# Optimization experiments

Hardware: AMD Instinct MI355X
Metric: run time of the kernel (lower is better)

## Reference

```python
import jax, jax.numpy as jnp
import numpy as np

N_NODES = 50000
NUM_REL = 8
IN_DIM = 128
HID = 256
NUM_CLASSES = 2
E = 1600000
M = 200000
LN_EPS = 1e-5


def setup_inputs() -> dict:
    key = jax.random.key(0)
    ks = jax.random.split(key, 20)
    s = 0.05
    inp = {
        "x": jax.random.normal(ks[0], (N_NODES, IN_DIM), jnp.float32),
        "edge_index": jax.random.randint(ks[1], (2, E), 0, N_NODES, jnp.int32),
        "edge_type": jax.random.randint(ks[2], (E,), 0, NUM_REL, jnp.int32),
        "dec_edges": jax.random.randint(ks[3], (M, 2), 0, N_NODES, jnp.int32),
        # conv1
        "W1": jax.random.normal(ks[4], (NUM_REL, IN_DIM, HID), jnp.float32) * s,
        "root1": jax.random.normal(ks[5], (IN_DIM, HID), jnp.float32) * s,
        "b1": jnp.zeros((HID,), jnp.float32),
        # conv2
        "W2": jax.random.normal(ks[6], (NUM_REL, HID, HID), jnp.float32) * s,
        "root2": jax.random.normal(ks[7], (HID, HID), jnp.float32) * s,
        "b2": jnp.zeros((HID,), jnp.float32),
        # layernorms
        "ln1_g": jnp.ones((HID,), jnp.float32),
        "ln1_b": jnp.zeros((HID,), jnp.float32),
        "ln2_g": jnp.ones((HID,), jnp.float32),
        "ln2_b": jnp.zeros((HID,), jnp.float32),
        # edge MLP: 2*HID -> HID -> HID//2 -> NUM_CLASSES
        "mlp_w1": jax.random.normal(ks[8], (2 * HID, HID), jnp.float32) * s,
        "mlp_b1": jnp.zeros((HID,), jnp.float32),
        "mlp_w2": jax.random.normal(ks[9], (HID, HID // 2), jnp.float32) * s,
        "mlp_b2": jnp.zeros((HID // 2,), jnp.float32),
        "mlp_w3": jax.random.normal(ks[10], (HID // 2, NUM_CLASSES), jnp.float32) * s,
        "mlp_b3": jnp.zeros((NUM_CLASSES,), jnp.float32),
    }
    return inp


def layer_norm(h, g, b):
    mu = jnp.mean(h, axis=-1, keepdims=True)
    var = jnp.mean(jnp.square(h - mu), axis=-1, keepdims=True)
    return (h - mu) * jax.lax.rsqrt(var + LN_EPS) * g + b


def rgcn_conv(x, edge_index, edge_type, W, root, bias):
    # PyG RGCNConv with aggr='mean': per-relation mean aggregation of
    # neighbor features, aggregate-then-transform (valid since linear),
    # plus root transform and bias.
    src, dst = edge_index[0], edge_index[1]
    xs = x[src]  # [E, d_in]
    out = x @ root + bias
    num_rel = W.shape[0]
    for r in range(num_rel):
        m = (edge_type == r).astype(x.dtype)  # [E]
        agg = jax.ops.segment_sum(xs * m[:, None], dst, num_segments=x.shape[0])
        cnt = jax.ops.segment_sum(m, dst, num_segments=x.shape[0])
        out = out + (agg / jnp.maximum(cnt, 1.0)[:, None]) @ W[r]
    return out


def reference(x, edge_index, edge_type, dec_edges,
              W1, root1, b1, W2, root2, b2,
              ln1_g, ln1_b, ln2_g, ln2_b,
              mlp_w1, mlp_b1, mlp_w2, mlp_b2, mlp_w3, mlp_b3):
    # encode (dropout is identity in eval mode)
    h1 = rgcn_conv(x, edge_index, edge_type, W1, root1, b1)
    h1 = layer_norm(jax.nn.relu(h1), ln1_g, ln1_b)
    h2 = rgcn_conv(h1, edge_index, edge_type, W2, root2, b2)
    h2 = layer_norm(jax.nn.relu(h2), ln2_g, ln2_b)
    h = h1 + h2
    # decode: gather endpoints, concat, MLP (exact-erf GELU as nn.GELU)
    z = jnp.concatenate([h[dec_edges[:, 0]], h[dec_edges[:, 1]]], axis=1)
    z = jax.nn.gelu(z @ mlp_w1 + mlp_b1, approximate=False)
    z = jax.nn.gelu(z @ mlp_w2 + mlp_b2, approximate=False)
    return z @ mlp_w3 + mlp_b3
```

## Files before the change

kernel.cpp:

```cpp
#include <hip/hip_runtime.h>
#include <math.h>

typedef __attribute__((ext_vector_type(8))) short short8;
typedef __attribute__((ext_vector_type(4))) float f32x4;
typedef __attribute__((address_space(3))) void lds_void;
typedef const __attribute__((address_space(1))) void glb_void;

#define N_NODES 50000
#define NUM_REL 8
#define IN_DIM 128
#define HID 256
#define E_EDGES 1600000
#define M_DEC 200000
#define K1 1152
#define K2 2304
#define LN_EPS 1e-5f
#define NSEG (N_NODES * 8)
#define NB2 782
#define SA_WG 391
#define SA_CH 4096
#define SA_DCH 512

#define RFL(x) __builtin_amdgcn_readfirstlane(x)

__device__ __forceinline__ float b2f(ushort u) {
    union { unsigned int i; float f; } v; v.i = ((unsigned int)u) << 16; return v.f;
}
__device__ __forceinline__ ushort f2b(float f) {
    union { float f; unsigned int i; } v; v.f = f;
    unsigned int r = v.i + 0x7FFFu + ((v.i >> 16) & 1u);
    return (ushort)(r >> 16);
}
__device__ __forceinline__ unsigned int pk2(ushort a, ushort b) {
    return (unsigned int)a | ((unsigned int)b << 16);
}
__device__ __forceinline__ float gelu_fast(float x) {
    float y = 1.5957691216f * (x + 0.044715f * x * x * x);
    float e = __expf(y);
    float t = 1.f - 2.f * __builtin_amdgcn_rcpf(e + 1.f);
    return 0.5f * x * (1.f + t);
}
__device__ __forceinline__ int clampn(int v) {
    if ((unsigned)v >= N_NODES) v = (v < 0) ? 0 : N_NODES - 1;
    return v;
}


__global__ __launch_bounds__(256) void coarse_count(const int* __restrict__ ei,
                                                    const int* __restrict__ dec,
                                                    int* __restrict__ bh, int* __restrict__ dh) {
    __shared__ int lb[NB2], ld[NB2];
    const int t = threadIdx.x;
    for (int i = t; i < NB2; i += 256) { lb[i] = 0; ld[i] = 0; }
    __syncthreads();
    const int e0 = blockIdx.x * SA_CH;
#pragma unroll
    for (int k = 0; k < 16; ++k) {
        int e = e0 + k * 256 + t;
        if (e < E_EDGES) {
            int dst = clampn(ei[E_EDGES + e]);
            atomicAdd(&lb[dst >> 6], 1);
        }
    }
    const int d0 = blockIdx.x * SA_DCH;
#pragma unroll
    for (int k = 0; k < 2; ++k) {
        int i = d0 + k * 256 + t;
        if (i < M_DEC) {
            int a = clampn(dec[(size_t)i * 2]);
            atomicAdd(&ld[a >> 6], 1);
        }
    }
    __syncthreads();
    for (int i = t; i < NB2; i += 256) {
        if (lb[i]) atomicAdd(&bh[i], lb[i]);
        if (ld[i]) atomicAdd(&dh[i], ld[i]);
    }
}

__global__ __launch_bounds__(1024) void scan_buckets(const int* __restrict__ bh, int* __restrict__ bbase,
                                                     int* __restrict__ bcur,
                                                     const int* __restrict__ dh, int* __restrict__ dbase,
                                                     int* __restrict__ dcur, int* __restrict__ rp2) {
    __shared__ int ts[1024];
    const int t = threadIdx.x;
    const int* src = (blockIdx.x == 0) ? bh : dh;
    int* ob = (blockIdx.x == 0) ? bbase : dbase;
    int* oc = (blockIdx.x == 0) ? bcur : dcur;
    int v = (t < NB2) ? src[t] : 0;
    ts[t] = v;
    __syncthreads();
#pragma unroll
    for (int off = 1; off < 1024; off <<= 1) {
        int u = (t >= off) ? ts[t - off] : 0;
        __syncthreads();
        ts[t] += u;
        __syncthreads();
    }
    if (t < NB2) { int ex = ts[t] - v; ob[t] = ex; oc[t] = ex; }
    if (t == NB2 - 1) ob[NB2] = ts[t];
    if (t == 0 && blockIdx.x == 0) rp2[NSEG] = E_EDGES;
}

__global__ __launch_bounds__(256) void stageA(const int* __restrict__ ei, const int* __restrict__ et,
                                              int* __restrict__ bcur, unsigned int* __restrict__ sbuf,
                                              const int* __restrict__ dec, int* __restrict__ dcur,
                                              int* __restrict__ perm) {
    __shared__ int h[NB2], base_[NB2];
    const int t = threadIdx.x;
    const int e0 = blockIdx.x * SA_CH;
    for (int i = t; i < NB2; i += 256) h[i] = 0;
    __syncthreads();
    int myb[16];
#pragma unroll
    for (int k = 0; k < 16; ++k) {
        int e = e0 + k * 256 + t;
        int b = -1;
        if (e < E_EDGES) {
            int dst = clampn(ei[E_EDGES + e]);
            b = dst >> 6;
            atomicAdd(&h[b], 1);
        }
        myb[k] = b;
    }
    __syncthreads();
    for (int i = t; i < NB2; i += 256) {
        int c = h[i];
        base_[i] = c ? atomicAdd(&bcur[i], c) : 0;
    }
    __syncthreads();
    for (int i = t; i < NB2; i += 256) h[i] = 0;
    __syncthreads();
#pragma unroll
    for (int k = 0; k < 16; ++k) {
        int e = e0 + k * 256 + t;
        int b = myb[k];
        if (b >= 0) {
            int dst = clampn(ei[E_EDGES + e]);
            int src = clampn(ei[e]);
            int r = et[e] & 7;
            int off = atomicAdd(&h[b], 1);
            sbuf[base_[b] + off] =
                (unsigned)src | ((unsigned)r << 16) | ((unsigned)(dst & 63) << 19);
        }
    }
    __syncthreads();
    for (int i = t; i < NB2; i += 256) h[i] = 0;
    __syncthreads();
    const int d0 = blockIdx.x * SA_DCH;
    int dbk[2];
#pragma unroll
    for (int k = 0; k < 2; ++k) {
        int i = d0 + k * 256 + t;
        int b = -1;
        if (i < M_DEC) {
            int a = clampn(dec[(size_t)i * 2]);
            b = a >> 6;
            atomicAdd(&h[b], 1);
        }
        dbk[k] = b;
    }
    __syncthreads();
    for (int i = t; i < NB2; i += 256) {
        int c = h[i];
        base_[i] = c ? atomicAdd(&dcur[i], c) : 0;
    }
    __syncthreads();
    for (int i = t; i < NB2; i += 256) h[i] = 0;
    __syncthreads();
#pragma unroll
    for (int k = 0; k < 2; ++k) {
        int i = d0 + k * 256 + t;
        int b = dbk[k];
        if (b >= 0) {
            int off = atomicAdd(&h[b], 1);
            perm[base_[b] + off] = i;
        }
    }
}

__global__ __launch_bounds__(512) void stageB(const unsigned int* __restrict__ sbuf,
                                              const int* __restrict__ bbase,
                                              int* __restrict__ rp2,
                                              unsigned int* __restrict__ epk) {
    __shared__ int cnt[512];
    __shared__ int pref[512];
    const int t = threadIdx.x;
    const int b = blockIdx.x;
    const int s0 = bbase[b], s1 = bbase[b + 1];
    cnt[t] = 0;
    __syncthreads();
    for (int i = s0 + t; i < s1; i += 512) {
        unsigned int p = sbuf[i];
        int ls = (((p >> 19) & 63) << 3) | ((p >> 16) & 7);
        atomicAdd(&cnt[ls], 1);
    }
    __syncthreads();
    pref[t] = cnt[t];
    __syncthreads();
#pragma unroll
    for (int off = 1; off < 512; off <<= 1) {
        int u = (t >= off) ? pref[t - off] : 0;
        __syncthreads();
        pref[t] += u;
        __syncthreads();
    }
    int excl = pref[t] - cnt[t];
    int seg = b * 512 + t;
    if (seg < NSEG) rp2[seg] = s0 + excl;
    __syncthreads();
    pref[t] = excl;
    cnt[t] = 0;
    __syncthreads();
    for (int i = s0 + t; i < s1; i += 512) {
        unsigned int p = sbuf[i];
        int ls = (((p >> 19) & 63) << 3) | ((p >> 16) & 7);
        int off = atomicAdd(&cnt[ls], 1);
        epk[s0 + pref[ls] + off] = p & 0xFFFFu;
    }
}

__global__ void pack_all(const float* __restrict__ x, ushort* __restrict__ xb,
                         const float* __restrict__ root1, const float* __restrict__ W1,
                         const float* __restrict__ root2, const float* __restrict__ W2,
                         ushort* __restrict__ B1t, ushort* __restrict__ B2t,
                         const float* __restrict__ mw1, const float* __restrict__ mw2,
                         ushort* __restrict__ wuvt, ushort* __restrict__ w2t) {
    const int XC = N_NODES * IN_DIM / 4;
    const int N1 = HID * K1;
    const int N2 = HID * K2;
    const int NU = 512 * 256;
    const int NW = 128 * 256;
    int idx = blockIdx.x * 256 + threadIdx.x;
    if (idx < XC) {
        float4 v = *(const float4*)(x + (size_t)idx * 4);
        uint2 o;
        o.x = pk2(f2b(v.x), f2b(v.y));
        o.y = pk2(f2b(v.z), f2b(v.w));
        *(uint2*)(xb + (size_t)idx * 4) = o;
        return;
    }
    idx -= XC;
    if (idx < N1) {
        int n = idx / K1, k = idx % K1;
        float v;
        if (k < IN_DIM) v = root1[k * HID + n];
        else { int kk = k - IN_DIM; v = W1[(size_t)(kk >> 7) * IN_DIM * HID + (kk & 127) * HID + n]; }
        B1t[(size_t)n * K1 + k] = f2b(v);
        return;
    }
    idx -= N1;
    if (idx < N2) {
        int n = idx / K2, k = idx % K2;
        float v;
        if (k < HID) v = root2[k * HID + n];
        else { int kk = k - HID; v = W2[(size_t)(kk >> 8) * HID * HID + (kk & 255) * HID + n]; }
        B2t[(size_t)n * K2 + k] = f2b(v);
        return;
    }
    idx -= N2;
    if (idx < NU) {
        int n = idx / 256, k = idx % 256;
        float v = (n < 256) ? mw1[(size_t)k * 256 + n] : mw1[(size_t)(256 + k) * 256 + (n - 256)];
        wuvt[(size_t)n * 256 + k] = f2b(v);
        return;
    }
    idx -= NU;
    if (idx < NW) {
        int n = idx / 256, k = idx % 256;
        w2t[n * 256 + k] = f2b(mw2[k * 128 + n]);
    }
}


#define FL1() { int c_ = segend - segbeg; float inv_ = c_ > 0 ? 1.f / (float)c_ : 0.f; \
    *(unsigned int*)(Arow + IN_DIM + r * IN_DIM + 2 * lane) = \
        pk2(f2b((aA.x + aB.x) * inv_), f2b((aA.y + aB.y) * inv_)); \
    aA.x = 0.f; aA.y = 0.f; aB.x = 0.f; aB.y = 0.f; \
    ++r; segbeg = segend; segend = (r < 8) ? RFL(rp[r + 1]) : end; \
    if (segend < segbeg) segend = segbeg; if (segend > end) segend = end; }
#define CK1(EI) { while (r < 8 && (EI) >= segend) FL1(); }
#define AC1A(U) { aA.x += b2f((ushort)((U) & 0xFFFFu)); aA.y += b2f((ushort)((U) >> 16)); }
#define AC1B(U) { aB.x += b2f((ushort)((U) & 0xFFFFu)); aB.y += b2f((ushort)((U) >> 16)); }

__global__ __launch_bounds__(256) void agg1_kernel(const ushort* __restrict__ xb,
                                                   const int* __restrict__ rp2,
                                                   const unsigned int* __restrict__ epk,
                                                   ushort* __restrict__ Achunk, int n0, int m) {
    const int w = threadIdx.x >> 6, lane = threadIdx.x & 63;
    const int local = blockIdx.x * 4 + w;
    if (local >= m) return;
    const int n = n0 + local;
    const int* rp = rp2 + n * 8;
    ushort* Arow = Achunk + (size_t)local * K1;
    const ushort* xbb = xb + 2 * lane;
    *(unsigned int*)(Arow + 2 * lane) = *(const unsigned int*)(xb + (size_t)n * IN_DIM + 2 * lane);

    int beg = RFL(rp[0]), end = RFL(rp[8]);
    if (beg < 0) beg = 0;
    if (end > E_EDGES) end = E_EDGES;
    if (end < beg) end = beg;

    float2 aA = {0.f, 0.f}, aB = {0.f, 0.f};
    int r = 0, segbeg = beg, segend = RFL(rp[1]);
    if (segend < segbeg) segend = segbeg; if (segend > end) segend = end;

    int e = beg;
    for (; e + 7 < end; e += 8) {
        unsigned int p0 = RFL(epk[e]),     p1 = RFL(epk[e + 1]);
        unsigned int p2 = RFL(epk[e + 2]), p3 = RFL(epk[e + 3]);
        unsigned int p4 = RFL(epk[e + 4]), p5 = RFL(epk[e + 5]);
        unsigned int p6 = RFL(epk[e + 6]), p7 = RFL(epk[e + 7]);
        unsigned int u0 = *(const unsigned int*)(xbb + (size_t)p0 * IN_DIM);
        unsigned int u1 = *(const unsigned int*)(xbb + (size_t)p1 * IN_DIM);
        unsigned int u2 = *(const unsigned int*)(xbb + (size_t)p2 * IN_DIM);
        unsigned int u3 = *(const unsigned int*)(xbb + (size_t)p3 * IN_DIM);
        unsigned int u4 = *(const unsigned int*)(xbb + (size_t)p4 * IN_DIM);
        unsigned int u5 = *(const unsigned int*)(xbb + (size_t)p5 * IN_DIM);
        unsigned int u6 = *(const unsigned int*)(xbb + (size_t)p6 * IN_DIM);
        unsigned int u7 = *(const unsigned int*)(xbb + (size_t)p7 * IN_DIM);
        CK1(e)     AC1A(u0) CK1(e + 1) AC1B(u1)
        CK1(e + 2) AC1A(u2) CK1(e + 3) AC1B(u3)
        CK1(e + 4) AC1A(u4) CK1(e + 5) AC1B(u5)
        CK1(e + 6) AC1A(u6) CK1(e + 7) AC1B(u7)
    }
    for (; e < end; ++e) {
        unsigned int p = RFL(epk[e]);
        unsigned int u = *(const unsigned int*)(xbb + (size_t)p * IN_DIM);
        CK1(e) AC1A(u)
    }
    while (r < 8) FL1();
}

#define FL2() { int c_ = segend - segbeg; float inv_ = c_ > 0 ? 1.f / (float)c_ : 0.f; \
    f32x4 t_ = aA + aB; uint2 o_; \
    o_.x = pk2(f2b(t_[0] * inv_), f2b(t_[1] * inv_)); \
    o_.y = pk2(f2b(t_[2] * inv_), f2b(t_[3] * inv_)); \
    *(uint2*)(Arow + HID + r * HID + 4 * lane) = o_; \
    aA = (f32x4){0.f, 0.f, 0.f, 0.f}; aB = aA; \
    ++r; segbeg = segend; segend = (r < 8) ? RFL(rp[r + 1]) : end; \
    if (segend < segbeg) segend = segbeg; if (segend > end) segend = end; }
#define CK2(EI) { while (r < 8 && (EI) >= segend) FL2(); }
#define AC2A(U) { f32x4 f_; \
    f_[0] = b2f((ushort)((U).x & 0xFFFFu)); f_[1] = b2f((ushort)((U).x >> 16)); \
    f_[2] = b2f((ushort)((U).y & 0xFFFFu)); f_[3] = b2f((ushort)((U).y >> 16)); aA += f_; }
#define AC2B(U) { f32x4 f_; \
    f_[0] = b2f((ushort)((U).x & 0xFFFFu)); f_[1] = b2f((ushort)((U).x >> 16)); \
    f_[2] = b2f((ushort)((U).y & 0xFFFFu)); f_[3] = b2f((ushort)((U).y >> 16)); aB += f_; }

__global__ __launch_bounds__(256) void agg2_kernel(const ushort* __restrict__ h1,
                                                   const int* __restrict__ rp2,
                                                   const unsigned int* __restrict__ epk,
                                                   ushort* __restrict__ Achunk, int n0, int m) {
    const int w = threadIdx.x >> 6, lane = threadIdx.x & 63;
    const int local = blockIdx.x * 4 + w;
    if (local >= m) return;
    const int n = n0 + local;
    const int* rp = rp2 + n * 8;
    ushort* Arow = Achunk + (size_t)local * K2;
    const ushort* hb = h1 + 4 * lane;
    *(uint2*)(Arow + 4 * lane) = *(const uint2*)(h1 + (size_t)n * HID + 4 * lane);

    int beg = RFL(rp[0]), end = RFL(rp[8]);
    if (beg < 0) beg = 0;
    if (end > E_EDGES) end = E_EDGES;
    if (end < beg) end = beg;

    f32x4 aA = {0.f, 0.f, 0.f, 0.f}, aB = {0.f, 0.f, 0.f, 0.f};
    int r = 0, segbeg = beg, segend = RFL(rp[1]);
    if (segend < segbeg) segend = segbeg; if (segend > end) segend = end;

    int e = beg;
    for (; e + 7 < end; e += 8) {
        unsigned int p0 = RFL(epk[e]),     p1 = RFL(epk[e + 1]);
        unsigned int p2 = RFL(epk[e + 2]), p3 = RFL(epk[e + 3]);
        unsigned int p4 = RFL(epk[e + 4]), p5 = RFL(epk[e + 5]);
        unsigned int p6 = RFL(epk[e + 6]), p7 = RFL(epk[e + 7]);
        uint2 u0 = *(const uint2*)(hb + (size_t)p0 * HID);
        uint2 u1 = *(const uint2*)(hb + (size_t)p1 * HID);
        uint2 u2 = *(const uint2*)(hb + (size_t)p2 * HID);
        uint2 u3 = *(const uint2*)(hb + (size_t)p3 * HID);
        uint2 u4 = *(const uint2*)(hb + (size_t)p4 * HID);
        uint2 u5 = *(const uint2*)(hb + (size_t)p5 * HID);
        uint2 u6 = *(const uint2*)(hb + (size_t)p6 * HID);
        uint2 u7 = *(const uint2*)(hb + (size_t)p7 * HID);
        CK2(e)     AC2A(u0) CK2(e + 1) AC2B(u1)
        CK2(e + 2) AC2A(u2) CK2(e + 3) AC2B(u3)
        CK2(e + 4) AC2A(u4) CK2(e + 5) AC2B(u5)
        CK2(e + 6) AC2A(u6) CK2(e + 7) AC2B(u7)
    }
    for (; e < end; ++e) {
        unsigned int p = RFL(epk[e]);
        uint2 u = *(const uint2*)(hb + (size_t)p * HID);
        CK2(e) AC2A(u)
    }
    while (r < 8) FL2();
}


#define STAGE(BUF, KO) { \
    __builtin_amdgcn_global_load_lds((glb_void*)(Ab + (KO)), \
        (lds_void*)(AsBase + (BUF) * 4096 + wave * 8 * 64), 16, 0, 0); \
    _Pragma("unroll") \
    for (int j_ = 0; j_ < 4; ++j_) \
        __builtin_amdgcn_global_load_lds((glb_void*)(Bb + (size_t)j_ * 8 * K + (KO)), \
            (lds_void*)(BsBase + (BUF) * 16384 + (wave * 32 + j_ * 8) * 64), 16, 0, 0); }

#define COMPUTE(CUR) { \
    _Pragma("unroll") \
    for (int kk = 0; kk < 2; ++kk) { \
        const int gsw = (((kk * 4 + qd) ^ (cc & 7)) * 8); \
        short8 af[2], bfv[4]; \
        _Pragma("unroll") \
        for (int i = 0; i < 2; ++i) \
            af[i] = *(const short8*)&AsBase[(CUR) * 4096 + (mh * 32 + i * 16 + cc) * 64 + gsw]; \
        _Pragma("unroll") \
        for (int j = 0; j < 4; ++j) \
            bfv[j] = *(const short8*)&BsBase[(CUR) * 16384 + (wn + j * 16 + cc) * 64 + gsw]; \
        _Pragma("unroll") \
        for (int i = 0; i < 2; ++i) \
            _Pragma("unroll") \
            for (int j = 0; j < 4; ++j) \
                acc[i][j] = __builtin_amdgcn_mfma_f32_16x16x32_bf16(af[i], bfv[j], acc[i][j], 0, 0, 0); \
    } }

__global__ __launch_bounds__(512, 4) void gemm_fused(
    const ushort* __restrict__ A, const ushort* __restrict__ Bt,
    int lda, int M, int K,
    const float* __restrict__ bias, const float* __restrict__ g,
    const float* __restrict__ bvec, const ushort* __restrict__ resid,
    ushort* __restrict__ outp, int ldc, int rowOff) {
    __shared__ __align__(16) ushort smem[40960];
    ushort* AsBase = smem;
    ushort* BsBase = smem + 2 * 64 * 64;
    const int tid = threadIdx.x;
    const int wave = tid >> 6, lane = tid & 63;
    const int w4 = wave & 3, mh = wave >> 2;
    const int cc = lane & 15, qd = lane >> 4;
    const int row0 = blockIdx.x * 64;
    const int colBase = blockIdx.y * 256;
    const int wn = w4 * 64;
    const int srow = lane >> 3;
    const int sgrp = (lane & 7) ^ (srow & 7);
    f32x4 acc[2][4];
#pragma unroll
    for (int i = 0; i < 2; ++i)
#pragma unroll
        for (int j = 0; j < 4; ++j) acc[i][j] = (f32x4){0.f, 0.f, 0.f, 0.f};

    const ushort* Ab = A + (size_t)(row0 + wave * 8 + srow) * lda + sgrp * 8;
    const ushort* Bb = Bt + (size_t)(colBase + wave * 32 + srow) * K + sgrp * 8;

    STAGE(0, 0)
    for (int k0 = 0; k0 < K; k0 += 128) {
        if (k0 + 64 < K) {
            STAGE(1, k0 + 64)
            asm volatile("s_waitcnt vmcnt(5)" ::: "memory");
        } else {
            asm volatile("s_waitcnt vmcnt(0)" ::: "memory");
        }
        __builtin_amdgcn_s_barrier();
        COMPUTE(0)
        asm volatile("s_waitcnt lgkmcnt(0)" ::: "memory");
        __builtin_amdgcn_s_barrier();

        if (k0 + 128 < K) {
            STAGE(0, k0 + 128)
            asm volatile("s_waitcnt vmcnt(5)" ::: "memory");
        } else {
            asm volatile("s_waitcnt vmcnt(0)" ::: "memory");
        }
        __builtin_amdgcn_s_barrier();
        COMPUTE(1)
        asm volatile("s_waitcnt lgkmcnt(0)" ::: "memory");
        __builtin_amdgcn_s_barrier();
    }

    if (g) {
        float* partS = (float*)smem;
        float* partQ = (float*)smem + 256;
        float* muS   = (float*)smem + 512;
        float* rsS   = (float*)smem + 576;
#pragma unroll
        for (int j = 0; j < 4; ++j) {
            float bcol = bias[wn + j * 16 + cc];
#pragma unroll
            for (int i = 0; i < 2; ++i)
#pragma unroll
                for (int r = 0; r < 4; ++r)
                    acc[i][j][r] = fmaxf(acc[i][j][r] + bcol, 0.f);
        }
#pragma unroll
        for (int i = 0; i < 2; ++i)
#pragma unroll
            for (int r = 0; r < 4; ++r) {
                float s = acc[i][0][r] + acc[i][1][r] + acc[i][2][r] + acc[i][3][r];
                float q = acc[i][0][r] * acc[i][0][r] + acc[i][1][r] * acc[i][1][r]
                        + acc[i][2][r] * acc[i][2][r] + acc[i][3][r] * acc[i][3][r];
#pragma unroll
                for (int off = 1; off <= 8; off <<= 1) {
                    s += __shfl_xor(s, off, 64);
                    q += __shfl_xor(q, off, 64);
                }
                if (cc == 0) {
                    int row = mh * 32 + i * 16 + qd * 4 + r;
                    partS[row * 4 + w4] = s;
                    partQ[row * 4 + w4] = q;
                }
            }
        __syncthreads();
        if (tid < 64) {
            float S = partS[tid * 4] + partS[tid * 4 + 1] + partS[tid * 4 + 2] + partS[tid * 4 + 3];
            float Q = partQ[tid * 4] + partQ[tid * 4 + 1] + partQ[tid * 4 + 2] + partQ[tid * 4 + 3];
            float mu = S * (1.f / 256.f);
            float var = Q * (1.f / 256.f) - mu * mu;
            muS[tid] = mu;
            rsS[tid] = rsqrtf(fmaxf(var, 0.f) + LN_EPS);
        }
        __syncthreads();
#pragma unroll
        for (int i = 0; i < 2; ++i)
#pragma unroll
            for (int r = 0; r < 4; ++r) {
                int row = mh * 32 + i * 16 + qd * 4 + r;
                int grow = row0 + row;
                if (grow >= M) continue;
                float mu = muS[row], rs = rsS[row];
                size_t base = (size_t)(rowOff + grow) * ldc;
#pragma unroll
                for (int j = 0; j < 4; ++j) {
                    int col = wn + j * 16 + cc;
                    float val = (acc[i][j][r] - mu) * rs * g[col] + bvec[col];
                    if (resid) val += b2f(resid[base + col]);
                    outp[base + col] = f2b(val);
                }
            }
    } else {
#pragma unroll
        for (int i = 0; i < 2; ++i)
#pragma unroll
            for (int r = 0; r < 4; ++r) {
                int grow = row0 + mh * 32 + i * 16 + qd * 4 + r;
                if (grow >= M) continue;
                size_t base = (size_t)(rowOff + grow) * ldc;
#pragma unroll
                for (int j = 0; j < 4; ++j) {
                    int col = colBase + wn + j * 16 + cc;
                    outp[base + col] = f2b(acc[i][j][r]);
                }
            }
    }
}

__global__ __launch_bounds__(256) void edge_kernel(
    const ushort* __restrict__ uv, const int* __restrict__ dec, const int* __restrict__ perm,
    const float* __restrict__ b1, const ushort* __restrict__ w2t,
    const float* __restrict__ b2, const float* __restrict__ w3,
    const float* __restrict__ b3, float* __restrict__ outp, int M) {
    __shared__ __align__(16) ushort z1s[64][264];
    __shared__ __align__(16) ushort z2s[64][136];
    __shared__ float b1s[256], b2s[128], w3s[256];
    __shared__ float part3[64][2][2];
    const int tid = threadIdx.x;
    const int wave = tid >> 6, lane = tid & 63;
    const int cc = lane & 15, qd = lane >> 4, lk = qd * 8, rr = qd * 4;
    const int e0 = blockIdx.x * 64;

    b1s[tid] = b1[tid];
    if (tid < 128) b2s[tid] = b2[tid];
    w3s[tid] = w3[tid];
    __syncthreads();

    {
        int e = tid >> 2, seg = tid & 3;
        int ge = perm[e0 + e];
        if (ge < 0) ge = 0; if (ge >= M) ge = M - 1;
        int a = dec[(size_t)ge * 2];
        int b = dec[(size_t)ge * 2 + 1];
        if (a < 0) a = 0; if (a >= N_NODES) a = N_NODES - 1;
        if (b < 0) b = 0; if (b >= N_NODES) b = N_NODES - 1;
        const ushort* up = uv + (size_t)a * 512 + seg * 64;
        const ushort* vp = uv + (size_t)b * 512 + 256 + seg * 64;
        short8 us[8], vs[8];
#pragma unroll
        for (int j = 0; j < 8; ++j) us[j] = *(const short8*)(up + j * 8);
#pragma unroll
        for (int j = 0; j < 8; ++j) vs[j] = *(const short8*)(vp + j * 8);
        int d0 = seg * 64;
#pragma unroll
        for (int j = 0; j < 8; ++j) {
            int d = d0 + j * 8;
            short8 zs;
#pragma unroll
            for (int l = 0; l < 8; ++l) {
                float z = b2f((ushort)us[j][l]) + b2f((ushort)vs[j][l]) + b1s[d + l];
                zs[l] = (short)f2b(gelu_fast(z));
            }
            *(short8*)&z1s[e][d] = zs;
        }
    }
    __syncthreads();

    f32x4 acc[4][2];
#pragma unroll
    for (int i = 0; i < 4; ++i)
#pragma unroll
        for (int j = 0; j < 2; ++j) acc[i][j] = (f32x4){0.f, 0.f, 0.f, 0.f};
    const int n0 = wave * 32;
#pragma unroll
    for (int ks = 0; ks < 8; ++ks) {
        short8 af[4], bfv[2];
#pragma unroll
        for (int i = 0; i < 4; ++i) af[i] = *(const short8*)&z1s[i * 16 + cc][ks * 32 + lk];
#pragma unroll
        for (int j = 0; j < 2; ++j)
            bfv[j] = *(const short8*)(w2t + (size_t)(n0 + j * 16 + cc) * 256 + ks * 32 + lk);
#pragma unroll
        for (int i = 0; i < 4; ++i)
#pragma unroll
            for (int j = 0; j < 2; ++j)
                acc[i][j] = __builtin_amdgcn_mfma_f32_16x16x32_bf16(af[i], bfv[j], acc[i][j], 0, 0, 0);
    }
#pragma unroll
    for (int i = 0; i < 4; ++i)
#pragma unroll
        for (int j = 0; j < 2; ++j)
#pragma unroll
            for (int r = 0; r < 4; ++r) {
                int m = i * 16 + rr + r;
                int n = n0 + j * 16 + cc;
                z2s[m][n] = f2b(gelu_fast(acc[i][j][r] + b2s[n]));
            }
    __syncthreads();

    {
        int e = tid >> 2, c = tid & 1, hf = (tid >> 1) & 1;
        const ushort* zr = &z2s[e][hf * 64];
        float s = 0.f;
#pragma unroll
        for (int j = 0; j < 8; ++j) {
            short8 v = *(const short8*)(zr + j * 8);
#pragma unroll
            for (int l = 0; l < 8; ++l)
                s += b2f((ushort)v[l]) * w3s[(hf * 64 + j * 8 + l) * 2 + c];
        }
        part3[e][c][hf] = s;
    }
    __syncthreads();
    if (tid < 128) {
        int e = tid >> 1, c = tid & 1;
        float s = part3[e][c][0] + part3[e][c][1] + b3[c];
        int ge = perm[e0 + e];
        if (ge >= 0 && ge < M) outp[(size_t)ge * 2 + c] = s;
    }
}

extern "C" void kernel_launch(void* const* d_in, const int* in_sizes, int n_in,
                              void* d_out, int out_size, void* d_ws, size_t ws_size,
                              hipStream_t stream) {
    const float* x          = (const float*)d_in[0];
    const int*   edge_index = (const int*)d_in[1];
    const int*   edge_type  = (const int*)d_in[2];
    const int*   dec_edges  = (const int*)d_in[3];
    const float* W1         = (const float*)d_in[4];
    const float* root1      = (const float*)d_in[5];
    const float* b1         = (const float*)d_in[6];
    const float* W2         = (const float*)d_in[7];
    const float* root2      = (const float*)d_in[8];
    const float* b2         = (const float*)d_in[9];
    const float* ln1_g      = (const float*)d_in[10];
    const float* ln1_b      = (const float*)d_in[11];
    const float* ln2_g      = (const float*)d_in[12];
    const float* ln2_b      = (const float*)d_in[13];
    const float* mlp_w1     = (const float*)d_in[14];
    const float* mlp_b1     = (const float*)d_in[15];
    const float* mlp_w2     = (const float*)d_in[16];
    const float* mlp_b2     = (const float*)d_in[17];
    const float* mlp_w3     = (const float*)d_in[18];
    const float* mlp_b3     = (const float*)d_in[19];

    char* ws = (char*)d_ws;
    size_t off = 0;
    auto alloc = [&](size_t bytes) {
        void* p = ws + off;
        off += (bytes + 255) & ~(size_t)255;
        return p;
    };
    unsigned int* epk     = (unsigned int*)alloc((size_t)E_EDGES * 4);
    unsigned int* sbuf    = (unsigned int*)alloc((size_t)E_EDGES * 4);
    int*          rp2     = (int*)alloc((size_t)(NSEG + 1) * 4);
    int*          hz      = (int*)alloc((size_t)2 * NB2 * 4);
    int*          bh      = hz;
    int*          dh      = hz + NB2;
    int*          bbase   = (int*)alloc((size_t)(NB2 + 1) * 4);
    int*          dbase   = (int*)alloc((size_t)(NB2 + 1) * 4);
    int*          bcur    = (int*)alloc((size_t)NB2 * 4);
    int*          dcur    = (int*)alloc((size_t)NB2 * 4);
    int*          perm    = (int*)alloc((size_t)M_DEC * 4);
    ushort*       B1t     = (ushort*)alloc((size_t)HID * K1 * 2);
    ushort*       B2t     = (ushort*)alloc((size_t)HID * K2 * 2);
    ushort*       wuvt    = (ushort*)alloc((size_t)512 * 256 * 2);
    ushort*       w2t     = (ushort*)alloc((size_t)128 * 256 * 2);
    ushort*       xb      = (ushort*)alloc((size_t)N_NODES * IN_DIM * 2);
    ushort*       hfin    = (ushort*)alloc((size_t)N_NODES * HID * 2);

    size_t regionOff = off;
    ushort* h1ln  = (ushort*)(ws + regionOff);
    ushort* uvbuf = h1ln;
    size_t h1b = (((size_t)N_NODES * HID * 2) + 255) & ~(size_t)255;
    ushort* Achunk = (ushort*)(ws + regionOff + h1b);
    long long chunkB = (long long)ws_size - (long long)(regionOff + h1b);
    int chunk = 64;
    if (chunkB > 0) {
        long long c = chunkB / ((long long)K2 * 2);
        if (c > N_NODES) c = N_NODES;
        c &= ~63LL;
        if (c >= 64) chunk = (int)c;
    }
    int chunk1 = chunk * 2;
    if (chunk1 > N_NODES) chunk1 = N_NODES;

    hipMemsetAsync(hz, 0, (size_t)2 * NB2 * 4, stream);
    coarse_count<<<SA_WG, 256, 0, stream>>>(edge_index, dec_edges, bh, dh);
    scan_buckets<<<2, 1024, 0, stream>>>(bh, bbase, bcur, dh, dbase, dcur, rp2);
    stageA<<<SA_WG, 256, 0, stream>>>(edge_index, edge_type, bcur, sbuf, dec_edges, dcur, perm);
    stageB<<<NB2, 512, 0, stream>>>(sbuf, bbase, rp2, epk);

    {
        int total = N_NODES * IN_DIM / 4 + HID * K1 + HID * K2 + 512 * 256 + 128 * 256;
        pack_all<<<(total + 255) / 256, 256, 0, stream>>>(x, xb, root1, W1, root2, W2,
                                                          B1t, B2t, mlp_w1, mlp_w2, wuvt, w2t);
    }

    for (int n0 = 0; n0 < N_NODES; n0 += chunk1) {
        int m = N_NODES - n0; if (m > chunk1) m = chunk1;
        agg1_kernel<<<(m + 3) / 4, 256, 0, stream>>>(xb, rp2, epk, Achunk, n0, m);
        gemm_fused<<<dim3((m + 63) / 64, 1), 512, 0, stream>>>(
            Achunk, B1t, K1, m, K1, b1, ln1_g, ln1_b, nullptr, h1ln, HID, n0);
    }
    for (int n0 = 0; n0 < N_NODES; n0 += chunk) {
        int m = N_NODES - n0; if (m > chunk) m = chunk;
        agg2_kernel<<<(m + 3) / 4, 256, 0, stream>>>(h1ln, rp2, epk, Achunk, n0, m);
        gemm_fused<<<dim3((m + 63) / 64, 1), 512, 0, stream>>>(
            Achunk, B2t, K2, m, K2, b2, ln2_g, ln2_b, h1ln, hfin, HID, n0);
    }

    gemm_fused<<<dim3((N_NODES + 63) / 64, 2), 512, 0, stream>>>(
        hfin, wuvt, HID, N_NODES, HID, nullptr, nullptr, nullptr, nullptr, uvbuf, 512, 0);

    edge_kernel<<<(M_DEC + 63) / 64, 256, 0, stream>>>(
        uvbuf, dec_edges, perm, mlp_b1, w2t, mlp_b2, mlp_w3, mlp_b3, (float*)d_out, M_DEC);
}
```

Before: 704.0 us.

## Double GEMM row tile to 128 so each B tile is reused across two A tiles

The fused GEMM now computes 128 rows per workgroup as two 64-row groups with separate accumulators. Each staged 64-column B tile is used by both groups, which halves B traffic per output row and halves the grid size. The load pipeline is rebuilt so A stages are interleaved with compute and B is prefetched two steps ahead, and A row indices are clamped at M. The cost is doubled accumulator registers and fewer workgroups, which may reduce occupancy and parallelism on small chunks.

```diff
diff --git a/kernel.cpp b/kernel.cpp
--- a/kernel.cpp
+++ b/kernel.cpp
@@ -398,30 +398,32 @@
 }
 
 
-#define STAGE(BUF, KO) { \
-    __builtin_amdgcn_global_load_lds((glb_void*)(Ab + (KO)), \
-        (lds_void*)(AsBase + (BUF) * 4096 + wave * 8 * 64), 16, 0, 0); \
+#define STAGEB(BUF, KO) { \
     _Pragma("unroll") \
     for (int j_ = 0; j_ < 4; ++j_) \
         __builtin_amdgcn_global_load_lds((glb_void*)(Bb + (size_t)j_ * 8 * K + (KO)), \
             (lds_void*)(BsBase + (BUF) * 16384 + (wave * 32 + j_ * 8) * 64), 16, 0, 0); }
 
-#define COMPUTE(CUR) { \
+#define STAGEA(G, PTR, KO) { \
+    __builtin_amdgcn_global_load_lds((glb_void*)((PTR) + (KO)), \
+        (lds_void*)(AsBase + (G) * 4096 + wave * 8 * 64), 16, 0, 0); }
+
+#define COMPUTEG(ACC, G, CB) { \
     _Pragma("unroll") \
     for (int kk = 0; kk < 2; ++kk) { \
         const int gsw = (((kk * 4 + qd) ^ (cc & 7)) * 8); \
         short8 af[2], bfv[4]; \
         _Pragma("unroll") \
         for (int i = 0; i < 2; ++i) \
-            af[i] = *(const short8*)&AsBase[(CUR) * 4096 + (mh * 32 + i * 16 + cc) * 64 + gsw]; \
+            af[i] = *(const short8*)&AsBase[(G) * 4096 + (mh * 32 + i * 16 + cc) * 64 + gsw]; \
         _Pragma("unroll") \
         for (int j = 0; j < 4; ++j) \
-            bfv[j] = *(const short8*)&BsBase[(CUR) * 16384 + (wn + j * 16 + cc) * 64 + gsw]; \
+            bfv[j] = *(const short8*)&BsBase[(CB) * 16384 + (wn + j * 16 + cc) * 64 + gsw]; \
         _Pragma("unroll") \
         for (int i = 0; i < 2; ++i) \
             _Pragma("unroll") \
             for (int j = 0; j < 4; ++j) \
-                acc[i][j] = __builtin_amdgcn_mfma_f32_16x16x32_bf16(af[i], bfv[j], acc[i][j], 0, 0, 0); \
+                ACC[i][j] = __builtin_amdgcn_mfma_f32_16x16x32_bf16(af[i], bfv[j], ACC[i][j], 0, 0, 0); \
     } }
 
 __global__ __launch_bounds__(512, 4) void gemm_fused(
@@ -437,79 +439,92 @@
     const int wave = tid >> 6, lane = tid & 63;
     const int w4 = wave & 3, mh = wave >> 2;
     const int cc = lane & 15, qd = lane >> 4;
-    const int row0 = blockIdx.x * 64;
+    const int row0 = blockIdx.x * 128;
     const int colBase = blockIdx.y * 256;
     const int wn = w4 * 64;
     const int srow = lane >> 3;
     const int sgrp = (lane & 7) ^ (srow & 7);
-    f32x4 acc[2][4];
+    f32x4 acc0[2][4], acc1[2][4];
 #pragma unroll
     for (int i = 0; i < 2; ++i)
 #pragma unroll
-        for (int j = 0; j < 4; ++j) acc[i][j] = (f32x4){0.f, 0.f, 0.f, 0.f};
-
-    const ushort* Ab = A + (size_t)(row0 + wave * 8 + srow) * lda + sgrp * 8;
+        for (int j = 0; j < 4; ++j) {
+            acc0[i][j] = (f32x4){0.f, 0.f, 0.f, 0.f};
+            acc1[i][j] = (f32x4){0.f, 0.f, 0.f, 0.f};
+        }
+
+    int rowA0 = row0 + wave * 8 + srow;       if (rowA0 >= M) rowA0 = M - 1;
+    int rowA1 = row0 + 64 + wave * 8 + srow;  if (rowA1 >= M) rowA1 = M - 1;
+    const ushort* Ab0 = A + (size_t)rowA0 * lda + sgrp * 8;
+    const ushort* Ab1 = A + (size_t)rowA1 * lda + sgrp * 8;
     const ushort* Bb = Bt + (size_t)(colBase + wave * 32 + srow) * K + sgrp * 8;
 
-    STAGE(0, 0)
-    for (int k0 = 0; k0 < K; k0 += 128) {
-        if (k0 + 64 < K) {
-            STAGE(1, k0 + 64)
-            asm volatile("s_waitcnt vmcnt(5)" ::: "memory");
-        } else {
-            asm volatile("s_waitcnt vmcnt(0)" ::: "memory");
-        }
+    const int NT = K >> 6;
+    STAGEB(0, 0)
+    STAGEA(0, Ab0, 0)
+    STAGEA(1, Ab1, 0)
+    if (NT > 1) STAGEB(1, 64)
+
+    for (int t = 0; t < NT; ++t) {
+        const int ko = t << 6;
+        const int cb = t & 1;
+        if (t + 1 < NT) { asm volatile("s_waitcnt vmcnt(5)" ::: "memory"); }
+        else           { asm volatile("s_waitcnt vmcnt(1)" ::: "memory"); }
         __builtin_amdgcn_s_barrier();
-        COMPUTE(0)
+        COMPUTEG(acc0, 0, cb)
         asm volatile("s_waitcnt lgkmcnt(0)" ::: "memory");
         __builtin_amdgcn_s_barrier();
-
-        if (k0 + 128 < K) {
-            STAGE(0, k0 + 128)
-            asm volatile("s_waitcnt vmcnt(5)" ::: "memory");
-        } else {
-            asm volatile("s_waitcnt vmcnt(0)" ::: "memory");
-        }
+        if (t + 1 < NT) STAGEA(0, Ab0, ko + 64)
+        if (t + 1 < NT) { asm volatile("s_waitcnt vmcnt(5)" ::: "memory"); }
+        else           { asm volatile("s_waitcnt vmcnt(0)" ::: "memory"); }
         __builtin_amdgcn_s_barrier();
-        COMPUTE(1)
+        COMPUTEG(acc1, 1, cb)
         asm volatile("s_waitcnt lgkmcnt(0)" ::: "memory");
         __builtin_amdgcn_s_barrier();
+        if (t + 1 < NT) {
+            STAGEA(1, Ab1, ko + 64)
+            if (t + 2 < NT) STAGEB(cb, ko + 128)
+        }
     }
 
     if (g) {
         float* partS = (float*)smem;
-        float* partQ = (float*)smem + 256;
-        float* muS   = (float*)smem + 512;
-        float* rsS   = (float*)smem + 576;
-#pragma unroll
-        for (int j = 0; j < 4; ++j) {
-            float bcol = bias[wn + j * 16 + cc];
+        float* partQ = (float*)smem + 512;
+        float* muS   = (float*)smem + 1024;
+        float* rsS   = (float*)smem + 1152;
+#pragma unroll
+        for (int gg = 0; gg < 2; ++gg) {
+            f32x4 (*ac)[4] = gg ? acc1 : acc0;
+#pragma unroll
+            for (int j = 0; j < 4; ++j) {
+                float bcol = bias[wn + j * 16 + cc];
+#pragma unroll
+                for (int i = 0; i < 2; ++i)
+#pragma unroll
+                    for (int r = 0; r < 4; ++r)
+                        ac[i][j][r] = fmaxf(ac[i][j][r] + bcol, 0.f);
+            }
 #pragma unroll
             for (int i = 0; i < 2; ++i)
 #pragma unroll
-                for (int r = 0; r < 4; ++r)
-                    acc[i][j][r] = fmaxf(acc[i][j][r] + bcol, 0.f);
-        }
-#pragma unroll
-        for (int i = 0; i < 2; ++i)
-#pragma unroll
-            for (int r = 0; r < 4; ++r) {
-                float s = acc[i][0][r] + acc[i][1][r] + acc[i][2][r] + acc[i][3][r];
-                float q = acc[i][0][r] * acc[i][0][r] + acc[i][1][r] * acc[i][1][r]
-                        + acc[i][2][r] * acc[i][2][r] + acc[i][3][r] * acc[i][3][r];
-#pragma unroll
-                for (int off = 1; off <= 8; off <<= 1) {
-                    s += __shfl_xor(s, off, 64);
-                    q += __shfl_xor(q, off, 64);
+                for (int r = 0; r < 4; ++r) {
+                    float s = ac[i][0][r] + ac[i][1][r] + ac[i][2][r] + ac[i][3][r];
+                    float q = ac[i][0][r] * ac[i][0][r] + ac[i][1][r] * ac[i][1][r]
+                            + ac[i][2][r] * ac[i][2][r] + ac[i][3][r] * ac[i][3][r];
+#pragma unroll
+                    for (int off = 1; off <= 8; off <<= 1) {
+                        s += __shfl_xor(s, off, 64);
+                        q += __shfl_xor(q, off, 64);
+                    }
+                    if (cc == 0) {
+                        int row = gg * 64 + mh * 32 + i * 16 + qd * 4 + r;
+                        partS[row * 4 + w4] = s;
+                        partQ[row * 4 + w4] = q;
+                    }
                 }
-                if (cc == 0) {
-                    int row = mh * 32 + i * 16 + qd * 4 + r;
-                    partS[row * 4 + w4] = s;
-                    partQ[row * 4 + w4] = q;
-                }
-            }
+        }
         __syncthreads();
-        if (tid < 64) {
+        if (tid < 128) {
             float S = partS[tid * 4] + partS[tid * 4 + 1] + partS[tid * 4 + 2] + partS[tid * 4 + 3];
             float Q = partQ[tid * 4] + partQ[tid * 4 + 1] + partQ[tid * 4 + 2] + partQ[tid * 4 + 3];
             float mu = S * (1.f / 256.f);
@@ -519,36 +534,44 @@
         }
         __syncthreads();
 #pragma unroll
-        for (int i = 0; i < 2; ++i)
-#pragma unroll
-            for (int r = 0; r < 4; ++r) {
-                int row = mh * 32 + i * 16 + qd * 4 + r;
-                int grow = row0 + row;
-                if (grow >= M) continue;
-                float mu = muS[row], rs = rsS[row];
-                size_t base = (size_t)(rowOff + grow) * ldc;
-#pragma unroll
-                for (int j = 0; j < 4; ++j) {
-                    int col = wn + j * 16 + cc;
-                    float val = (acc[i][j][r] - mu) * rs * g[col] + bvec[col];
-                    if (resid) val += b2f(resid[base + col]);
-                    outp[base + col] = f2b(val);
+        for (int gg = 0; gg < 2; ++gg) {
+            f32x4 (*ac)[4] = gg ? acc1 : acc0;
+#pragma unroll
+            for (int i = 0; i < 2; ++i)
+#pragma unroll
+                for (int r = 0; r < 4; ++r) {
+                    int row = gg * 64 + mh * 32 + i * 16 + qd * 4 + r;
+                    int grow = row0 + row;
+                    if (grow >= M) continue;
+                    float mu = muS[row], rs = rsS[row];
+                    size_t base = (size_t)(rowOff + grow) * ldc;
+#pragma unroll
+                    for (int j = 0; j < 4; ++j) {
+                        int col = wn + j * 16 + cc;
+                        float val = (ac[i][j][r] - mu) * rs * g[col] + bvec[col];
+                        if (resid) val += b2f(resid[base + col]);
+                        outp[base + col] = f2b(val);
+                    }
                 }
-            }
+        }
     } else {
 #pragma unroll
-        for (int i = 0; i < 2; ++i)
-#pragma unroll
-            for (int r = 0; r < 4; ++r) {
-                int grow = row0 + mh * 32 + i * 16 + qd * 4 + r;
-                if (grow >= M) continue;
-                size_t base = (size_t)(rowOff + grow) * ldc;
-#pragma unroll
-                for (int j = 0; j < 4; ++j) {
-                    int col = colBase + wn + j * 16 + cc;
-                    outp[base + col] = f2b(acc[i][j][r]);
+        for (int gg = 0; gg < 2; ++gg) {
+            f32x4 (*ac)[4] = gg ? acc1 : acc0;
+#pragma unroll
+            for (int i = 0; i < 2; ++i)
+#pragma unroll
+                for (int r = 0; r < 4; ++r) {
+                    int grow = row0 + gg * 64 + mh * 32 + i * 16 + qd * 4 + r;
+                    if (grow >= M) continue;
+                    size_t base = (size_t)(rowOff + grow) * ldc;
+#pragma unroll
+                    for (int j = 0; j < 4; ++j) {
+                        int col = colBase + wn + j * 16 + cc;
+                        outp[base + col] = f2b(ac[i][j][r]);
+                    }
                 }
-            }
+        }
     }
 }
 
@@ -735,17 +758,17 @@
     for (int n0 = 0; n0 < N_NODES; n0 += chunk1) {
         int m = N_NODES - n0; if (m > chunk1) m = chunk1;
         agg1_kernel<<<(m + 3) / 4, 256, 0, stream>>>(xb, rp2, epk, Achunk, n0, m);
-        gemm_fused<<<dim3((m + 63) / 64, 1), 512, 0, stream>>>(
+        gemm_fused<<<dim3((m + 127) / 128, 1), 512, 0, stream>>>(
             Achunk, B1t, K1, m, K1, b1, ln1_g, ln1_b, nullptr, h1ln, HID, n0);
     }
     for (int n0 = 0; n0 < N_NODES; n0 += chunk) {
         int m = N_NODES - n0; if (m > chunk) m = chunk;
         agg2_kernel<<<(m + 3) / 4, 256, 0, stream>>>(h1ln, rp2, epk, Achunk, n0, m);
-        gemm_fused<<<dim3((m + 63) / 64, 1), 512, 0, stream>>>(
+        gemm_fused<<<dim3((m + 127) / 128, 1), 512, 0, stream>>>(
             Achunk, B2t, K2, m, K2, b2, ln2_g, ln2_b, h1ln, hfin, HID, n0);
     }
 
-    gemm_fused<<<dim3((N_NODES + 63) / 64, 2), 512, 0, stream>>>(
+    gemm_fused<<<dim3((N_NODES + 127) / 128, 2), 512, 0, stream>>>(
         hfin, wuvt, HID, N_NODES, HID, nullptr, nullptr, nullptr, nullptr, uvbuf, 512, 0);
 
     edge_kernel<<<(M_DEC + 63) / 64, 256, 0, stream>>>(
```

Result: slower. 765.7 us (+8.8%).
